# Kernel optimization log

Hardware: AMD Instinct MI355X
Metric: run time of the kernel (lower is better)

The kernel has to match this reference:

```python
import jax, jax.numpy as jnp
import numpy as np


def gcn_conv(x, edge_index, edge_weight, W, b):
    """Faithful PyG GCNConv: add self-loops (weight 1), symmetric normalization,
    linear transform, weighted sum aggregation at target nodes, then bias."""
    N = x.shape[0]
    loops = jnp.arange(N, dtype=edge_index.dtype)
    row = jnp.concatenate([edge_index[0], loops])  # source j
    col = jnp.concatenate([edge_index[1], loops])  # target i
    ew = jnp.concatenate([edge_weight, jnp.ones((N,), dtype=edge_weight.dtype)])
    deg = jax.ops.segment_sum(ew, col, num_segments=N)  # [N]
    dinv = jnp.where(deg > 0, jax.lax.rsqrt(deg), 0.0)
    norm = dinv[row] * ew * dinv[col]  # [E+N]
    xw = x @ W  # [N, F_out]
    msgs = xw[row] * norm[:, None]  # [E+N, F_out]
    out = jax.ops.segment_sum(msgs, col, num_segments=N)  # [N, F_out]
    return out + b


def setup_inputs() -> dict:
    key = jax.random.key(0)
    k = jax.random.split(key, 8)
    N, E, Fin, Fhid, Fout = 50000, 800000, 128, 128, 64
    x = jax.random.normal(k[0], (N, Fin), dtype=jnp.float32)
    edge_index = jax.random.randint(k[1], (2, E), 0, N, dtype=jnp.int64)
    edge_weight = jax.random.uniform(k[2], (E,), dtype=jnp.float32)
    s0 = 1.0 / np.sqrt(Fin)
    s1 = 1.0 / np.sqrt(Fhid)
    W0 = jax.random.uniform(k[3], (Fin, Fhid), jnp.float32, -s0, s0)
    b0 = jnp.zeros((Fhid,), jnp.float32)
    W1 = jax.random.uniform(k[4], (Fhid, Fout), jnp.float32, -s1, s1)
    b1 = jnp.zeros((Fout,), jnp.float32)
    return {"x": x, "edge_index": edge_index, "edge_weight": edge_weight,
            "W0": W0, "b0": b0, "W1": W1, "b1": b1}


def reference(x, edge_index, edge_weight, W0, b0, W1, b1):
    # Encoder with num_layers=2, drop_p=0.0 (identity), activation=ReLU
    h = gcn_conv(x, edge_index, edge_weight, W0, b0)
    h = jax.nn.relu(h)
    h = gcn_conv(h, edge_index, edge_weight, W1, b1)
    h = jax.nn.relu(h)
    return h
```

## Files before the change

### kernel.cpp

```cpp
#include <hip/hip_runtime.h>

#define MAXDEG 48
#define BSH 6
#define BNODES 64
#define BCAP 2048

typedef unsigned short ushort_t;
typedef __attribute__((ext_vector_type(8))) short short8;
typedef __attribute__((ext_vector_type(4))) float f32x4;

__device__ inline ushort_t f2bf(float f) {
    union { float f; unsigned u; } v;
    v.f = f;
    unsigned r = v.u + 0x7fff + ((v.u >> 16) & 1);
    return (ushort_t)(r >> 16);
}

__device__ inline float bf2f_lo(unsigned u) {
    union { unsigned u; float f; } v;
    v.u = u << 16;
    return v.f;
}

__device__ inline float bf2f_hi(unsigned u) {
    union { unsigned u; float f; } v;
    v.u = u & 0xffff0000u;
    return v.f;
}


__global__ void k_setup(const float* __restrict__ W0, ushort_t* __restrict__ wp0,
                        const float* __restrict__ W1, ushort_t* __restrict__ wp1,
                        int* __restrict__ bcur, int NB) {
    int tid = blockIdx.x * blockDim.x + threadIdx.x;
    int stride = gridDim.x * blockDim.x;
    for (int i = tid; i < NB; i += stride) bcur[i] = 0;
    for (int e = tid; e < 16384; e += stride) {
        int j = e & 7, l = (e >> 3) & 63, ct = e >> 9;
        int t = ct & 7, c = ct >> 3;
        int k = 32 * c + (l >> 4) * 8 + j;
        int n = 16 * t + (l & 15);
        wp0[e] = f2bf(W0[k * 128 + n]);
    }
    for (int e = tid; e < 8192; e += stride) {
        int j = e & 7, l = (e >> 3) & 63, ct = e >> 9;
        int t = ct & 3, c = ct >> 2;
        int k = 32 * c + (l >> 4) * 8 + j;
        int n = 16 * t + (l & 15);
        wp1[e] = f2bf(W1[k * 64 + n]);
    }
}


__global__ __launch_bounds__(256) void k_scatter(const int* __restrict__ row,
                                                 const int* __restrict__ col,
                                                 const float* __restrict__ ew,
                                                 int* __restrict__ bcur,
                                                 uint2* __restrict__ recs, int E, int NB) {
    __shared__ int cnt[1024];
    __shared__ int base[1024];
    const int t = threadIdx.x;
    const size_t e0 = (size_t)blockIdx.x * (256 * 16);
    for (int i = t; i < NB; i += 256) cnt[i] = 0;
    __syncthreads();
    int ck[16], rk[16];
#pragma unroll
    for (int j = 0; j < 16; ++j) {
        size_t e = e0 + (size_t)j * 256 + t;
        ck[j] = -1;
        if (e < (size_t)E) {
            int c = col[e];
            ck[j] = c;
            rk[j] = atomicAdd(&cnt[c >> BSH], 1);
        }
    }
    __syncthreads();
    for (int i = t; i < NB; i += 256) {
        int c = cnt[i];
        base[i] = c ? atomicAdd(&bcur[i], c) : 0;
    }
    __syncthreads();
#pragma unroll
    for (int j = 0; j < 16; ++j) {
        size_t e = e0 + (size_t)j * 256 + t;
        if (e < (size_t)E) {
            int c = ck[j];
            int b = c >> BSH;
            int idx = base[b] + rk[j];
            if (idx < BCAP) {
                uint2 r;
                r.x = (unsigned)row[e] | ((unsigned)(c & (BNODES - 1)) << 16);
                r.y = __float_as_uint(ew[e]);
                recs[(size_t)b * BCAP + idx] = r;
            }
        }
    }
}


__global__ __launch_bounds__(256) void k_ell_build(const uint2* __restrict__ recs,
                                                   const int* __restrict__ bcur,
                                                   uint2* __restrict__ ell,
                                                   int* __restrict__ counts,
                                                   float* __restrict__ dinv, int N) {
    __shared__ uint2 tile[BNODES * MAXDEG];
    __shared__ int cnt[BNODES];
    const int b = blockIdx.x;
    const int t = threadIdx.x;
    if (t < BNODES) cnt[t] = 0;
    __syncthreads();
    const size_t s = (size_t)b * BCAP;
    const int ne = min(bcur[b], BCAP);
    for (int i = t; i < ne; i += 256) {
        uint2 r = recs[s + i];
        int dl = (r.x >> 16) & (BNODES - 1);
        int pos = atomicAdd(&cnt[dl], 1);
        if (pos < MAXDEG) {
            uint2 c;
            c.x = r.x & 0xffffu;
            c.y = r.y;
            tile[dl * MAXDEG + pos] = c;
        }
    }
    __syncthreads();
    const int node0 = b << BSH;
    if (t < BNODES) {
        int node = node0 + t;
        if (node < N) {
            int cn = min(cnt[t], MAXDEG);
            float sum = 1.0f;
            for (int j = 0; j < cn; ++j) sum += __uint_as_float(tile[t * MAXDEG + j].y);
            dinv[node] = rsqrtf(sum);
            counts[node] = cn;
        }
    }
    __syncthreads();
    const int nvalid = min(BNODES, N - node0);
    const int total = nvalid * MAXDEG;
    for (int i = t; i < total; i += 256) {
        int nl = i / MAXDEG;
        int slot = i - nl * MAXDEG;
        if (slot < min(cnt[nl], MAXDEG))
            ell[(size_t)node0 * MAXDEG + i] = tile[i];
    }
}


__global__ __launch_bounds__(256) void k_gemm1(const float* __restrict__ X,
                                               const uint4* __restrict__ Wp,
                                               ushort_t* __restrict__ Y, int N) {
    const int wave = threadIdx.x >> 6;
    const int lane = threadIdx.x & 63;
    const int m0 = blockIdx.x * 64 + wave * 16;
    if (m0 >= N) return;
    const int q = lane >> 4;
    const int mr = lane & 15;
    const int rowc = min(m0 + mr, N - 1);

    short8 a[4];
    const float* xr = X + (size_t)rowc * 128 + q * 8;
#pragma unroll
    for (int c = 0; c < 4; ++c) {
        float4 v0 = *(const float4*)(xr + 32 * c);
        float4 v1 = *(const float4*)(xr + 32 * c + 4);
        a[c][0] = (short)f2bf(v0.x); a[c][1] = (short)f2bf(v0.y);
        a[c][2] = (short)f2bf(v0.z); a[c][3] = (short)f2bf(v0.w);
        a[c][4] = (short)f2bf(v1.x); a[c][5] = (short)f2bf(v1.y);
        a[c][6] = (short)f2bf(v1.z); a[c][7] = (short)f2bf(v1.w);
    }

#pragma unroll
    for (int t = 0; t < 8; ++t) {
        f32x4 acc = {0.0f, 0.0f, 0.0f, 0.0f};
#pragma unroll
        for (int c = 0; c < 4; ++c) {
            uint4 bw = Wp[(size_t)(c * 8 + t) * 64 + lane];
            short8 b;
            __builtin_memcpy(&b, &bw, 16);
            acc = __builtin_amdgcn_mfma_f32_16x16x32_bf16(a[c], b, acc, 0, 0, 0);
        }
        const int colbase = 16 * t + mr;
#pragma unroll
        for (int r = 0; r < 4; ++r) {
            int orow = m0 + q * 4 + r;
            if (orow < N) Y[(size_t)orow * 128 + colbase] = f2bf(acc[r]);
        }
    }
}


__global__ __launch_bounds__(256) void k_gather128_gemm2(
        const int* __restrict__ counts, const uint2* __restrict__ ell,
        const float* __restrict__ dinv, const unsigned* __restrict__ xwb,
        const float* __restrict__ b0, const uint4* __restrict__ wp1,
        ushort_t* __restrict__ xw2b, int N) {
    __shared__ ushort_t h1[4][136];
    const int wave = threadIdx.x >> 6, lane = threadIdx.x & 63;
    const int node0 = blockIdx.x * 4;
    const int node = node0 + wave;

    unsigned packed = 0u;
    if (node < N) {
        float di = dinv[node];
        int cnt = min(counts[node], MAXDEG);
        int sv = 0;
        float wv = 0.0f;
        if (lane < cnt) {
            uint2 rec = ell[(size_t)node * MAXDEG + lane];
            sv = (int)rec.x;
            wv = dinv[sv] * __uint_as_float(rec.y) * di;
        }
        unsigned u0 = xwb[(size_t)node * 64 + lane];
        float2 bb = ((const float2*)b0)[lane];
        float sw = di * di;
        float ax = bb.x + bf2f_lo(u0) * sw;
        float ay = bb.y + bf2f_hi(u0) * sw;
        int j = 0;
        for (; j + 4 <= cnt; j += 4) {
            int s0 = __shfl(sv, j), s1 = __shfl(sv, j + 1),
                s2 = __shfl(sv, j + 2), s3 = __shfl(sv, j + 3);
            float w0 = __shfl(wv, j), w1 = __shfl(wv, j + 1),
                  w2 = __shfl(wv, j + 2), w3 = __shfl(wv, j + 3);
            unsigned v0 = xwb[(size_t)s0 * 64 + lane];
            unsigned v1 = xwb[(size_t)s1 * 64 + lane];
            unsigned v2 = xwb[(size_t)s2 * 64 + lane];
            unsigned v3 = xwb[(size_t)s3 * 64 + lane];
            ax += bf2f_lo(v0) * w0; ay += bf2f_hi(v0) * w0;
            ax += bf2f_lo(v1) * w1; ay += bf2f_hi(v1) * w1;
            ax += bf2f_lo(v2) * w2; ay += bf2f_hi(v2) * w2;
            ax += bf2f_lo(v3) * w3; ay += bf2f_hi(v3) * w3;
        }
        for (; j < cnt; ++j) {
            int s = __shfl(sv, j);
            float w = __shfl(wv, j);
            unsigned v = xwb[(size_t)s * 64 + lane];
            ax += bf2f_lo(v) * w; ay += bf2f_hi(v) * w;
        }
        packed = ((unsigned)f2bf(fmaxf(ay, 0.0f)) << 16) | f2bf(fmaxf(ax, 0.0f));
    }
    *(unsigned*)&h1[wave][2 * lane] = packed;
    __syncthreads();

    const int q = lane >> 4, mr = lane & 15;
    short8 a[4];
#pragma unroll
    for (int c = 0; c < 4; ++c)
        __builtin_memcpy(&a[c], &h1[mr & 3][32 * c + 8 * q], 16);
    f32x4 acc = {0.0f, 0.0f, 0.0f, 0.0f};
#pragma unroll
    for (int c = 0; c < 4; ++c) {
        uint4 bw = wp1[(size_t)(c * 4 + wave) * 64 + lane];
        short8 bf;
        __builtin_memcpy(&bf, &bw, 16);
        acc = __builtin_amdgcn_mfma_f32_16x16x32_bf16(a[c], bf, acc, 0, 0, 0);
    }
    if (q == 0) {
#pragma unroll
        for (int r = 0; r < 4; ++r) {
            int orow = node0 + r;
            if (orow < N) xw2b[(size_t)orow * 64 + 16 * wave + mr] = f2bf(acc[r]);
        }
    }
}


__global__ __launch_bounds__(256) void k_gather64_relu(const int* __restrict__ counts,
                                                       const uint2* __restrict__ ell,
                                                       const float* __restrict__ dinv,
                                                       const ushort_t* __restrict__ xwb,
                                                       const float* __restrict__ bias,
                                                       float* __restrict__ h, int N) {
    int node = (blockIdx.x * 256 + threadIdx.x) >> 6;
    int lane = threadIdx.x & 63;
    if (node >= N) return;
    float di = dinv[node];
    int cnt = min(counts[node], MAXDEG);

    int sv = 0;
    float wv = 0.0f;
    if (lane < cnt) {
        uint2 rec = ell[(size_t)node * MAXDEG + lane];
        sv = (int)rec.x;
        wv = dinv[sv] * __uint_as_float(rec.y) * di;
    }

    float acc = bias[lane] + bf2f_lo((unsigned)xwb[(size_t)node * 64 + lane]) * di * di;

    int j = 0;
    for (; j + 4 <= cnt; j += 4) {
        int s0 = __shfl(sv, j), s1 = __shfl(sv, j + 1), s2 = __shfl(sv, j + 2), s3 = __shfl(sv, j + 3);
        float w0 = __shfl(wv, j), w1 = __shfl(wv, j + 1), w2 = __shfl(wv, j + 2), w3 = __shfl(wv, j + 3);
        float v0 = bf2f_lo((unsigned)xwb[(size_t)s0 * 64 + lane]);
        float v1 = bf2f_lo((unsigned)xwb[(size_t)s1 * 64 + lane]);
        float v2 = bf2f_lo((unsigned)xwb[(size_t)s2 * 64 + lane]);
        float v3 = bf2f_lo((unsigned)xwb[(size_t)s3 * 64 + lane]);
        acc += v0 * w0 + v1 * w1 + v2 * w2 + v3 * w3;
    }
    for (; j < cnt; ++j) {
        acc += bf2f_lo((unsigned)xwb[(size_t)__shfl(sv, j) * 64 + lane]) * __shfl(wv, j);
    }
    h[(size_t)node * 64 + lane] = fmaxf(acc, 0.0f);
}


extern "C" void kernel_launch(void* const* d_in, const int* in_sizes, int n_in,
                              void* d_out, int out_size, void* d_ws, size_t ws_size,
                              hipStream_t stream) {
    const float* x  = (const float*)d_in[0];
    const int*   ei = (const int*)d_in[1];
    const float* ew = (const float*)d_in[2];
    const float* W0 = (const float*)d_in[3];
    const float* b0 = (const float*)d_in[4];
    const float* W1 = (const float*)d_in[5];
    const float* b1 = (const float*)d_in[6];
    float* out = (float*)d_out;

    const int Fhid = in_sizes[4];
    const int Fin  = in_sizes[3] / Fhid;
    const int N    = in_sizes[0] / Fin;
    const int E    = in_sizes[2];
    const int NB   = (N + BNODES - 1) >> BSH;

    const int* row = ei;
    const int* col = ei + E;

    char* w = (char*)d_ws;
    auto alloc = [&](size_t bytes) {
        char* p = w;
        w += (bytes + 255) & ~(size_t)255;
        return p;
    };
    float*    dinv   = (float*)alloc((size_t)N * 4);
    int*      counts = (int*)alloc((size_t)N * 4);
    int*      bcur   = (int*)alloc((size_t)NB * 4);
    uint2*    recs   = (uint2*)alloc((size_t)NB * BCAP * 8);
    uint2*    ell    = (uint2*)alloc((size_t)N * MAXDEG * 8);
    ushort_t* xw1b   = (ushort_t*)alloc((size_t)N * 128 * 2);
    ushort_t* xw2b   = (ushort_t*)alloc((size_t)N * 64 * 2);
    ushort_t* wp0    = (ushort_t*)alloc(16384 * 2);
    ushort_t* wp1    = (ushort_t*)alloc(8192 * 2);

    const int T = 256;
    const int GB = (N + 63) / 64;

    k_setup<<<32, T, 0, stream>>>(W0, wp0, W1, wp1, bcur, NB);
    k_scatter<<<(E + 4095) / 4096, T, 0, stream>>>(row, col, ew, bcur, recs, E, NB);
    k_ell_build<<<NB, T, 0, stream>>>(recs, bcur, ell, counts, dinv, N);
    k_gemm1<<<GB, T, 0, stream>>>(x, (const uint4*)wp0, xw1b, N);
    k_gather128_gemm2<<<(N + 3) / 4, T, 0, stream>>>(counts, ell, dinv,
                                                     (const unsigned*)xw1b, b0,
                                                     (const uint4*)wp1, xw2b, N);
    k_gather64_relu<<<(N + 3) / 4, T, 0, stream>>>(counts, ell, dinv, xw2b, b1, out, N);
}
```

Measured before the change: 190.1 us.

## Precompute normalized edge weights in ELL inside the first GEMM launch

Adds 2048 extra blocks to the first GEMM launch. They walk the ELL table and overwrite each edge weight with dinv[src]*w*dinv[dst]. Both gather kernels then read the stored normalized weight and no longer do the random dinv[src] lookup per edge. This trades one extra read-modify-write pass over the ELL array, which runs alongside the GEMM, for fewer dependent scattered loads in two gather kernels.

```diff
diff --git a/kernel.cpp b/kernel.cpp
--- a/kernel.cpp
+++ b/kernel.cpp
@@ -146,12 +146,12 @@
 }
 
 
-__global__ __launch_bounds__(256) void k_gemm1(const float* __restrict__ X,
-                                               const uint4* __restrict__ Wp,
-                                               ushort_t* __restrict__ Y, int N) {
+__device__ inline void gemm1_body(const float* __restrict__ X,
+                                  const uint4* __restrict__ Wp,
+                                  ushort_t* __restrict__ Y, int N, int g) {
     const int wave = threadIdx.x >> 6;
     const int lane = threadIdx.x & 63;
-    const int m0 = blockIdx.x * 64 + wave * 16;
+    const int m0 = g * 64 + wave * 16;
     if (m0 >= N) return;
     const int q = lane >> 4;
     const int mr = lane & 15;
@@ -184,6 +184,30 @@
         for (int r = 0; r < 4; ++r) {
             int orow = m0 + q * 4 + r;
             if (orow < N) Y[(size_t)orow * 128 + colbase] = f2bf(acc[r]);
+        }
+    }
+}
+
+
+__global__ __launch_bounds__(256) void k_gemm1_norm(
+        const float* __restrict__ X, const uint4* __restrict__ Wp,
+        ushort_t* __restrict__ Y, int N, int GB,
+        uint2* __restrict__ ell, const int* __restrict__ counts,
+        const float* __restrict__ dinv) {
+    if ((int)blockIdx.x < GB) {
+        gemm1_body(X, Wp, Y, N, blockIdx.x);
+        return;
+    }
+    const int nthreads = ((int)gridDim.x - GB) * 256;
+    int tid = ((int)blockIdx.x - GB) * 256 + threadIdx.x;
+    const int total = N * MAXDEG;
+    for (int i = tid; i < total; i += nthreads) {
+        int node = i / MAXDEG;
+        int slot = i - node * MAXDEG;
+        if (slot < min(counts[node], MAXDEG)) {
+            uint2 r = ell[i];
+            float wv = dinv[r.x] * __uint_as_float(r.y) * dinv[node];
+            ell[i].y = __float_as_uint(wv);
         }
     }
 }
@@ -208,7 +232,7 @@
         if (lane < cnt) {
             uint2 rec = ell[(size_t)node * MAXDEG + lane];
             sv = (int)rec.x;
-            wv = dinv[sv] * __uint_as_float(rec.y) * di;
+            wv = __uint_as_float(rec.y);
         }
         unsigned u0 = xwb[(size_t)node * 64 + lane];
         float2 bb = ((const float2*)b0)[lane];
@@ -281,7 +305,7 @@
     if (lane < cnt) {
         uint2 rec = ell[(size_t)node * MAXDEG + lane];
         sv = (int)rec.x;
-        wv = dinv[sv] * __uint_as_float(rec.y) * di;
+        wv = __uint_as_float(rec.y);
     }
 
     float acc = bias[lane] + bf2f_lo((unsigned)xwb[(size_t)node * 64 + lane]) * di * di;
@@ -346,7 +370,8 @@
     k_setup<<<32, T, 0, stream>>>(W0, wp0, W1, wp1, bcur, NB);
     k_scatter<<<(E + 4095) / 4096, T, 0, stream>>>(row, col, ew, bcur, recs, E, NB);
     k_ell_build<<<NB, T, 0, stream>>>(recs, bcur, ell, counts, dinv, N);
-    k_gemm1<<<GB, T, 0, stream>>>(x, (const uint4*)wp0, xw1b, N);
+    k_gemm1_norm<<<GB + 2048, T, 0, stream>>>(x, (const uint4*)wp0, xw1b, N, GB,
+                                              ell, counts, dinv);
     k_gather128_gemm2<<<(N + 3) / 4, T, 0, stream>>>(counts, ell, dinv,
                                                      (const unsigned*)xw1b, b0,
                                                      (const uint4*)wp1, xw2b, N);
```

Result: no change. 187.3 us (-1.5%).
